# Optimization experiments

Hardware: AMD Instinct MI355X
Metric: run time of the kernel (lower is better)

The kernel has to match this reference:

```python
import jax, jax.numpy as jnp
import numpy as np

B = 64          # number of jets
LVLS = 13       # tree levels (complete binary tree, 4096 leaves/jet)
F = 7           # input features
H = 64          # hidden size
SIZES = [B * (2 ** j) for j in range(LVLS)]
OFFS = np.concatenate([[0], np.cumsum(SIZES)])  # level offsets into flat contents


def setup_inputs() -> dict:
    key = jax.random.key(0)
    ks = jax.random.split(key, 9)
    n_total = int(OFFS[-1])  # 524224
    s = lambda k, shp, fan: jax.random.normal(k, shp, jnp.float32) / np.sqrt(fan)
    return {
        "contents": jax.random.normal(ks[0], (n_total, F), jnp.float32),
        "W_u": s(ks[1], (H, F), F),       "b_u": jnp.zeros((H,), jnp.float32),
        "W_r": s(ks[2], (3 * H, 3 * H), 3 * H), "b_r": jnp.zeros((3 * H,), jnp.float32),
        "W_h": s(ks[3], (H, 3 * H), 3 * H),     "b_h": jnp.zeros((H,), jnp.float32),
        "W_z": s(ks[4], (4 * H, 4 * H), 4 * H), "b_z": jnp.zeros((4 * H,), jnp.float32),
    }


def reference(contents, W_u, b_u, W_r, b_r, W_h, b_h, W_z, b_z):
    # Bottom-up recursive gated embedding (n_iters=0 path -> relu activation).
    up = None  # embedding of level j+1
    for j in reversed(range(LVLS)):
        c = contents[int(OFFS[j]):int(OFFS[j + 1])]        # [n_j, F]
        u = jax.nn.relu(c @ W_u.T + b_u)                   # [n_j, H]
        if j == LVLS - 1:
            up = u                                         # leaf level: no inners
            continue
        n = SIZES[j]
        # children of node k are (2k, 2k+1) at level j+1 -> strided gather
        h_L = up[0::2]                                     # [n_j, H]
        h_R = up[1::2]                                     # [n_j, H]
        hhu = jnp.concatenate([h_L, h_R, u], axis=1)       # [n_j, 3H]
        r = jax.nn.sigmoid(hhu @ W_r.T + b_r)              # reset gate
        h_H = jax.nn.relu((r * hhu) @ W_h.T + b_h)         # candidate
        z = jnp.concatenate([h_H, hhu], axis=1) @ W_z.T + b_z  # [n_j, 4H]
        g = jax.nn.softmax(z.reshape(n, 4, H), axis=1)     # softmax over 4 gates
        up = g[:, 0] * h_H + g[:, 1] * h_L + g[:, 2] * h_R + g[:, 3] * u
    return up.reshape(B, -1)                               # [B, H]
```

## Files before the change

kernel.cpp:

```cpp
#include <hip/hip_runtime.h>
#include <hip/hip_bf16.h>


#define LOG2E 1.4426950408889634f
#define OSTR 76

typedef __bf16 bf16x8 __attribute__((ext_vector_type(8)));
typedef unsigned short u16x8 __attribute__((ext_vector_type(8)));
typedef float f32x4 __attribute__((ext_vector_type(4)));
typedef unsigned short bfr;

__device__ __forceinline__ float bfr2f(bfr v) { return __uint_as_float(((unsigned)v) << 16); }
__device__ __forceinline__ bfr f2bfr(float f) {
    __hip_bfloat16 h = __float2bfloat16(f);
    return __builtin_bit_cast(bfr, h);
}
__device__ __forceinline__ float fexp2(float x) {
#if __has_builtin(__builtin_amdgcn_exp2f)
    return __builtin_amdgcn_exp2f(x);
#else
    return exp2f(x);
#endif
}
__device__ __forceinline__ float frcp(float x) {
#if __has_builtin(__builtin_amdgcn_rcpf)
    return __builtin_amdgcn_rcpf(x);
#else
    return 1.f / x;
#endif
}

__device__ __forceinline__ int fidx(int Mt, int kt, int q, int ln, int KT) {
    return ((((Mt * KT + kt) * 4 + q) * 16 + ln) * 8);
}

__device__ __host__ __forceinline__ size_t lvloff(int j) {
    return (size_t)((64 << j) - 64) * 64;
}

__device__ __forceinline__ void pack_one(const float* __restrict__ W, bfr* __restrict__ dst,
                                         int d, int K, float scale) {
    int KT = K >> 5;
    int j = d & 7, lnc = (d >> 3) & 15, q = (d >> 7) & 3;
    int t1 = d >> 9;
    int kt = t1 % KT, ntile = t1 / KT;
    int ncol = ntile * 16 + lnc;
    int k = kt * 32 + q * 8 + j;
    dst[d] = f2bfr(W[(size_t)ncol * K + k] * scale);
}

__global__ void convert_weights(const float* __restrict__ Wr, const float* __restrict__ Wh,
                                const float* __restrict__ Wz, const float* __restrict__ Wu,
                                const float* __restrict__ br, const float* __restrict__ bz,
                                bfr* __restrict__ wr, bfr* __restrict__ wh, bfr* __restrict__ wz,
                                bfr* __restrict__ wu,
                                float* __restrict__ brs, float* __restrict__ bzs) {
    int i = blockIdx.x * 256 + threadIdx.x;
    if (i < 36864) pack_one(Wr, wr, i, 192, LOG2E);
    if (i < 12288) pack_one(Wh, wh, i, 192, 1.f);
    if (i < 65536) pack_one(Wz, wz, i, 256, LOG2E);
    if (i < 2048) {
        int j = i & 7, lnc = (i >> 3) & 15, q = (i >> 7) & 3, ntile = i >> 9;
        int k = q * 8 + j, ncol = ntile * 16 + lnc;
        wu[i] = (k < 7) ? f2bfr(Wu[ncol * 7 + k]) : (bfr)0;
    }
    if (i < 192) brs[i] = br[i] * LOG2E;
    if (i < 256) bzs[i] = bz[i] * LOG2E;
}

__device__ __forceinline__ void stage_c(const float* __restrict__ csrc, int rows,
                                        bfr* s_c) {
    const int tid = threadIdx.x;
    for (int t = tid; t < rows * 4; t += 256) {
        int row = t >> 2, qg = t & 3;
        ushort v[8] = {0, 0, 0, 0, 0, 0, 0, 0};
        if (qg == 0) {
            const float* cp = csrc + (size_t)row * 7;
#pragma unroll
            for (int k = 0; k < 7; ++k) v[k] = f2bfr(cp[k]);
        }
        *(uint4*)&s_c[(((row >> 4) * 4 + qg) * 16 + (row & 15)) * 8] = *(const uint4*)v;
    }
}

__device__ __forceinline__ bf16x8 load_c_frag(const float* __restrict__ c,
                                              size_t grow, bool active) {
    u16x8 cv = {0, 0, 0, 0, 0, 0, 0, 0};
    if (active) {
        const float* cp = c + grow * 7;
#pragma unroll
        for (int k = 0; k < 7; ++k) cv[k] = f2bfr(cp[k]);
    }
    return __builtin_bit_cast(bf16x8, cv);
}

__device__ __forceinline__ void store_up_coalesced(
    int row0, int rows, bfr* __restrict__ u_io,
    const ushort (&ovv)[4][4], int Mtn, bfr* s_t)
{
    const int tid = threadIdx.x;
    const int lane = tid & 63, w = tid >> 6;
    const int ln = lane & 15, q = lane >> 4;
    const int colbase = w * 16 + q * 4;
    __syncthreads();
#pragma unroll
    for (int Mt = 0; Mt < 4; ++Mt) {
        if (Mt < Mtn) {
            int row = Mt * 16 + ln;
            if (row < rows)
                *(uint2*)&s_t[row * OSTR + colbase] = *(const uint2*)ovv[Mt];
        }
    }
    __syncthreads();
#pragma unroll
    for (int it = 0; it < 2; ++it) {
        int idx = it * 256 + tid;
        int row = idx >> 3, ck = idx & 7;
        if (row < rows)
            *(uint4*)&u_io[(size_t)(row0 + row) * 64 + ck * 8] =
                *(const uint4*)&s_t[row * OSTR + ck * 8];
    }
}

__device__ __forceinline__ void mmu_own(const bfr* s_c, bfr* s_hhu, bf16x8 awu,
                                        f32x4 bu4, int Mtn, int ln, int q,
                                        int colbase) {
#pragma unroll
    for (int Mt = 0; Mt < 4; ++Mt) {
        if (Mt < Mtn) {
            bf16x8 Bc = *(const bf16x8*)&s_c[((Mt * 4 + q) * 16 + ln) * 8];
            f32x4 acc = {0.f, 0.f, 0.f, 0.f};
            acc = __builtin_amdgcn_mfma_f32_16x16x32_bf16(awu, Bc, acc, 0, 0, 0);
            int kk = 128 + colbase;
            int addr = fidx(Mt, kk >> 5, (kk >> 3) & 3, ln, 6) + (kk & 7);
            ushort uv[4];
#pragma unroll
            for (int r = 0; r < 4; ++r) uv[r] = f2bfr(fmaxf(acc[r] + bu4[r], 0.f));
            *(uint2*)&s_hhu[addr] = *(const uint2*)uv;
        }
    }
}

template <bool CHILD_U>
__device__ __forceinline__ void tile_glob(
    int row0,
    const bfr* __restrict__ ch, const float* __restrict__ c_child,
    const float* __restrict__ c_own, bfr* __restrict__ u_io,
    const bfr* __restrict__ wu, const float* __restrict__ b_u,
    const bfr* __restrict__ wr, const float* __restrict__ brs,
    const bfr* __restrict__ wh, const float* __restrict__ b_h,
    const bfr* __restrict__ wz, const float* __restrict__ bzs,
    bfr* s_hhu, bfr* s_t)
{
    bfr* s_hH = s_t;
    const int tid = threadIdx.x;
    const int lane = tid & 63, w = tid >> 6;
    const int ln = lane & 15, q = lane >> 4;
    const int colbase = w * 16 + q * 4;

    if (!CHILD_U) {
#pragma unroll
        for (int it = 0; it < 4; ++it) {
            int idx = it * 256 + tid;
            int lns = idx & 15, qs = (idx >> 4) & 3, kts = (idx >> 6) & 3, Mts = idx >> 8;
            int row = Mts * 16 + lns;
            int k = kts * 32 + qs * 8;
            const bfr* src = (k < 64)
                ? ch + (size_t)(2 * (row0 + row)) * 64 + k
                : ch + (size_t)(2 * (row0 + row) + 1) * 64 + (k - 64);
            *(uint4*)&s_hhu[fidx(Mts, kts, qs, lns, 6)] = *(const uint4*)src;
        }
    } else {
        stage_c(c_child + (size_t)(2 * row0) * 7, 128, s_t + 2048);
    }
    stage_c(c_own + (size_t)row0 * 7, 64, s_t);
    __syncthreads();

    {
        bf16x8 awu = *(const bf16x8*)&wu[fidx(w, 0, q, ln, 1)];
        f32x4 bu4 = *(const f32x4*)&b_u[colbase];
        if (CHILD_U) {
#pragma unroll
            for (int Mt = 0; Mt < 8; ++Mt) {
                bf16x8 Bc = *(const bf16x8*)&s_t[2048 + (((Mt * 4 + q) * 16 + ln) * 8)];
                f32x4 acc = {0.f, 0.f, 0.f, 0.f};
                acc = __builtin_amdgcn_mfma_f32_16x16x32_bf16(awu, Bc, acc, 0, 0, 0);
                int crow = Mt * 16 + ln;
                int row = crow >> 1;
                int kk = (crow & 1) * 64 + colbase;
                int addr = fidx(row >> 4, kk >> 5, (kk >> 3) & 3, row & 15, 6) + (kk & 7);
                ushort uv[4];
#pragma unroll
                for (int r = 0; r < 4; ++r) uv[r] = f2bfr(fmaxf(acc[r] + bu4[r], 0.f));
                *(uint2*)&s_hhu[addr] = *(const uint2*)uv;
            }
        }
        mmu_own(s_t, s_hhu, awu, bu4, 4, ln, q, colbase);
    }
    __syncthreads();

    {
        bf16x8 Af[3][6];
#pragma unroll
        for (int nt = 0; nt < 3; ++nt)
#pragma unroll
            for (int kt = 0; kt < 6; ++kt)
                Af[nt][kt] = *(const bf16x8*)&wr[fidx(w * 3 + nt, kt, q, ln, 6)];
#pragma unroll
        for (int Mt = 0; Mt < 4; ++Mt) {
            bf16x8 Bf[6];
#pragma unroll
            for (int kt = 0; kt < 6; ++kt)
                Bf[kt] = *(const bf16x8*)&s_hhu[fidx(Mt, kt, q, ln, 6)];
#pragma unroll
            for (int nt = 0; nt < 3; ++nt) {
                int cb1 = (w * 3 + nt) * 16 + q * 4;
                f32x4 acc = {0.f, 0.f, 0.f, 0.f};
#pragma unroll
                for (int kt = 0; kt < 6; ++kt)
                    acc = __builtin_amdgcn_mfma_f32_16x16x32_bf16(Af[nt][kt], Bf[kt], acc, 0, 0, 0);
                f32x4 br4 = *(const f32x4*)&brs[cb1];
                int addr = fidx(Mt, cb1 >> 5, (cb1 >> 3) & 3, ln, 6) + (cb1 & 7);
                ushort hh[4], tt[4];
                *(uint2*)hh = *(const uint2*)&s_hhu[addr];
#pragma unroll
                for (int r = 0; r < 4; ++r) {
                    float e = fexp2(-(acc[r] + br4[r]));
                    tt[r] = f2bfr(frcp(1.f + e) * bfr2f(hh[r]));
                }
                *(uint2*)&s_t[addr] = *(const uint2*)tt;
            }
        }
    }
    __syncthreads();

    f32x4 hacc[4];
    {
        bf16x8 Ah[6];
#pragma unroll
        for (int kt = 0; kt < 6; ++kt)
            Ah[kt] = *(const bf16x8*)&wh[fidx(w, kt, q, ln, 6)];
#pragma unroll
        for (int Mt = 0; Mt < 4; ++Mt) {
            f32x4 acc = {0.f, 0.f, 0.f, 0.f};
#pragma unroll
            for (int kt = 0; kt < 6; ++kt) {
                bf16x8 Bf = *(const bf16x8*)&s_t[fidx(Mt, kt, q, ln, 6)];
                acc = __builtin_amdgcn_mfma_f32_16x16x32_bf16(Ah[kt], Bf, acc, 0, 0, 0);
            }
            hacc[Mt] = acc;
        }
    }
    __syncthreads();
    {
        f32x4 bh4 = *(const f32x4*)&b_h[colbase];
#pragma unroll
        for (int Mt = 0; Mt < 4; ++Mt) {
            int addr = fidx(Mt, colbase >> 5, (colbase >> 3) & 3, ln, 2) + (colbase & 7);
            ushort hv[4];
#pragma unroll
            for (int r = 0; r < 4; ++r) hv[r] = f2bfr(fmaxf(hacc[Mt][r] + bh4[r], 0.f));
            *(uint2*)&s_hH[addr] = *(const uint2*)hv;
        }
    }
    __syncthreads();

    {
        f32x4 az[4][4];
#pragma unroll
        for (int Mt = 0; Mt < 4; ++Mt)
#pragma unroll
            for (int g = 0; g < 4; ++g) az[Mt][g] = (f32x4){0.f, 0.f, 0.f, 0.f};
#pragma unroll
        for (int g = 0; g < 4; ++g) {
            bf16x8 Aw[8];
#pragma unroll
            for (int kt = 0; kt < 8; ++kt)
                Aw[kt] = *(const bf16x8*)&wz[fidx(g * 4 + w, kt, q, ln, 8)];
#pragma unroll
            for (int Mt = 0; Mt < 4; ++Mt) {
                f32x4 acc = az[Mt][g];
                acc = __builtin_amdgcn_mfma_f32_16x16x32_bf16(
                    Aw[0], *(const bf16x8*)&s_hH[fidx(Mt, 0, q, ln, 2)], acc, 0, 0, 0);
                acc = __builtin_amdgcn_mfma_f32_16x16x32_bf16(
                    Aw[1], *(const bf16x8*)&s_hH[fidx(Mt, 1, q, ln, 2)], acc, 0, 0, 0);
#pragma unroll
                for (int kt = 0; kt < 6; ++kt)
                    acc = __builtin_amdgcn_mfma_f32_16x16x32_bf16(
                        Aw[2 + kt], *(const bf16x8*)&s_hhu[fidx(Mt, kt, q, ln, 6)], acc, 0, 0, 0);
                az[Mt][g] = acc;
            }
        }
        f32x4 bz0 = *(const f32x4*)&bzs[colbase];
        f32x4 bz1 = *(const f32x4*)&bzs[64 + colbase];
        f32x4 bz2 = *(const f32x4*)&bzs[128 + colbase];
        f32x4 bz3 = *(const f32x4*)&bzs[192 + colbase];
        ushort ovv[4][4];
#pragma unroll
        for (int Mt = 0; Mt < 4; ++Mt) {
            int aH = fidx(Mt, colbase >> 5, (colbase >> 3) & 3, ln, 2) + (colbase & 7);
            int a0 = fidx(Mt, colbase >> 5, (colbase >> 3) & 3, ln, 6) + (colbase & 7);
            int c1 = 64 + colbase, c2 = 128 + colbase;
            int a1 = fidx(Mt, c1 >> 5, (c1 >> 3) & 3, ln, 6) + (c1 & 7);
            int a2 = fidx(Mt, c2 >> 5, (c2 >> 3) & 3, ln, 6) + (c2 & 7);
            ushort hHv[4], u0[4], u1[4], u2[4];
            *(uint2*)hHv = *(const uint2*)&s_hH[aH];
            *(uint2*)u0 = *(const uint2*)&s_hhu[a0];
            *(uint2*)u1 = *(const uint2*)&s_hhu[a1];
            *(uint2*)u2 = *(const uint2*)&s_hhu[a2];
#pragma unroll
            for (int r = 0; r < 4; ++r) {
                float e0 = fexp2(az[Mt][0][r] + bz0[r]);
                float e1 = fexp2(az[Mt][1][r] + bz1[r]);
                float e2 = fexp2(az[Mt][2][r] + bz2[r]);
                float e3 = fexp2(az[Mt][3][r] + bz3[r]);
                float inv = frcp(e0 + e1 + e2 + e3);
                float v = (e0 * bfr2f(hHv[r]) + e1 * bfr2f(u0[r]) +
                           e2 * bfr2f(u1[r]) + e3 * bfr2f(u2[r])) * inv;
                ovv[Mt][r] = f2bfr(v);
            }
        }
        store_up_coalesced(row0, 64, u_io, ovv, 4, s_t);
    }
}

__global__ __launch_bounds__(256, 2) void level11_kernel(
    const float* __restrict__ c12, const float* __restrict__ c11,
    bfr* __restrict__ u_io,
    const bfr* __restrict__ wr, const float* __restrict__ brs,
    const bfr* __restrict__ wh, const float* __restrict__ b_h,
    const bfr* __restrict__ wz, const float* __restrict__ bzs,
    const bfr* __restrict__ wu, const float* __restrict__ b_u)
{
    __shared__ bfr s_hhu[12288];
    __shared__ bfr s_t[12288];
    tile_glob<true>(blockIdx.x * 64, nullptr, c12, c11, u_io,
                    wu, b_u, wr, brs, wh, b_h, wz, bzs, s_hhu, s_t);
}

__global__ __launch_bounds__(256, 2) void level_kernel(
    const bfr* __restrict__ ch, const float* __restrict__ c_own,
    bfr* __restrict__ u_io,
    const bfr* __restrict__ wr, const float* __restrict__ brs,
    const bfr* __restrict__ wh, const float* __restrict__ b_h,
    const bfr* __restrict__ wz, const float* __restrict__ bzs,
    const bfr* __restrict__ wu, const float* __restrict__ b_u)
{
    __shared__ bfr s_hhu[12288];
    __shared__ bfr s_t[12288];
    tile_glob<false>(blockIdx.x * 64, ch, nullptr, c_own, u_io,
                     wu, b_u, wr, brs, wh, b_h, wz, bzs, s_hhu, s_t);
}

__device__ __forceinline__ void load_wregs(
    const bfr* __restrict__ wr, const bfr* __restrict__ wh, const bfr* __restrict__ wz,
    const bfr* __restrict__ wu, int w, int q, int ln,
    bf16x8 (&Af)[3][6], bf16x8 (&Ah)[6], bf16x8 (&Aw)[4][8], bf16x8& awu)
{
#pragma unroll
    for (int nt = 0; nt < 3; ++nt)
#pragma unroll
        for (int kt = 0; kt < 6; ++kt)
            Af[nt][kt] = *(const bf16x8*)&wr[fidx(w * 3 + nt, kt, q, ln, 6)];
#pragma unroll
    for (int kt = 0; kt < 6; ++kt)
        Ah[kt] = *(const bf16x8*)&wh[fidx(w, kt, q, ln, 6)];
#pragma unroll
    for (int g = 0; g < 4; ++g)
#pragma unroll
        for (int kt = 0; kt < 8; ++kt)
            Aw[g][kt] = *(const bf16x8*)&wz[fidx(g * 4 + w, kt, q, ln, 8)];
    awu = *(const bf16x8*)&wu[fidx(w, 0, q, ln, 1)];
}

__device__ __forceinline__ void tile_regs(
    int row0, int rows,
    const bfr* __restrict__ ch, const float* __restrict__ c_own,
    bfr* __restrict__ u_io,
    const bf16x8 awu, const float* __restrict__ b_u,
    const bf16x8 (&Af)[3][6], const bf16x8 (&Ah)[6], const bf16x8 (&Aw)[4][8],
    const float* __restrict__ brs, const float* __restrict__ b_h,
    const float* __restrict__ bzs,
    float* __restrict__ outp, bfr* s_hhu, bfr* s_t, bfr* s_hH)
{
    const int tid = threadIdx.x;
    const int lane = tid & 63, w = tid >> 6;
    const int ln = lane & 15, q = lane >> 4;
    const int Mtn = (rows + 15) >> 4;
    const int colbase = w * 16 + q * 4;

    __syncthreads();

#pragma unroll
    for (int it = 0; it < 4; ++it) {
        int idx = it * 256 + tid;
        int lns = idx & 15, qs = (idx >> 4) & 3, kts = (idx >> 6) & 3, Mts = idx >> 8;
        int row = Mts * 16 + lns;
        if (row < rows) {
            int k = kts * 32 + qs * 8;
            const bfr* src = (k < 64)
                ? ch + (size_t)(2 * (row0 + row)) * 64 + k
                : ch + (size_t)(2 * (row0 + row) + 1) * 64 + (k - 64);
            *(uint4*)&s_hhu[fidx(Mts, kts, qs, lns, 6)] = *(const uint4*)src;
        }
    }
    {
        f32x4 bu4 = *(const f32x4*)&b_u[colbase];
#pragma unroll
        for (int Mt = 0; Mt < 4; ++Mt) {
            if (Mt < Mtn) {
                int row = Mt * 16 + ln;
                bf16x8 Bc = load_c_frag(c_own, (size_t)row0 + row, q == 0 && row < rows);
                f32x4 acc = {0.f, 0.f, 0.f, 0.f};
                acc = __builtin_amdgcn_mfma_f32_16x16x32_bf16(awu, Bc, acc, 0, 0, 0);
                int kk = 128 + colbase;
                int addr = fidx(Mt, kk >> 5, (kk >> 3) & 3, ln, 6) + (kk & 7);
                ushort uv[4];
#pragma unroll
                for (int r = 0; r < 4; ++r) uv[r] = f2bfr(fmaxf(acc[r] + bu4[r], 0.f));
                *(uint2*)&s_hhu[addr] = *(const uint2*)uv;
            }
        }
    }
    __syncthreads();

#pragma unroll
    for (int Mt = 0; Mt < 4; ++Mt) {
        if (Mt < Mtn) {
            bf16x8 Bf[6];
#pragma unroll
            for (int kt = 0; kt < 6; ++kt)
                Bf[kt] = *(const bf16x8*)&s_hhu[fidx(Mt, kt, q, ln, 6)];
#pragma unroll
            for (int nt = 0; nt < 3; ++nt) {
                int cb1 = (w * 3 + nt) * 16 + q * 4;
                f32x4 acc = {0.f, 0.f, 0.f, 0.f};
#pragma unroll
                for (int kt = 0; kt < 6; ++kt)
                    acc = __builtin_amdgcn_mfma_f32_16x16x32_bf16(Af[nt][kt], Bf[kt], acc, 0, 0, 0);
                f32x4 br4 = *(const f32x4*)&brs[cb1];
                int addr = fidx(Mt, cb1 >> 5, (cb1 >> 3) & 3, ln, 6) + (cb1 & 7);
                ushort hh[4], tt[4];
                *(uint2*)hh = *(const uint2*)&s_hhu[addr];
#pragma unroll
                for (int r = 0; r < 4; ++r) {
                    float e = fexp2(-(acc[r] + br4[r]));
                    tt[r] = f2bfr(frcp(1.f + e) * bfr2f(hh[r]));
                }
                *(uint2*)&s_t[addr] = *(const uint2*)tt;
            }
        }
    }
    __syncthreads();

    {
        f32x4 bh4 = *(const f32x4*)&b_h[colbase];
#pragma unroll
        for (int Mt = 0; Mt < 4; ++Mt) {
            if (Mt < Mtn) {
                f32x4 acc = {0.f, 0.f, 0.f, 0.f};
#pragma unroll
                for (int kt = 0; kt < 6; ++kt) {
                    bf16x8 Bf = *(const bf16x8*)&s_t[fidx(Mt, kt, q, ln, 6)];
                    acc = __builtin_amdgcn_mfma_f32_16x16x32_bf16(Ah[kt], Bf, acc, 0, 0, 0);
                }
                int addr = fidx(Mt, colbase >> 5, (colbase >> 3) & 3, ln, 2) + (colbase & 7);
                ushort hv[4];
#pragma unroll
                for (int r = 0; r < 4; ++r) hv[r] = f2bfr(fmaxf(acc[r] + bh4[r], 0.f));
                *(uint2*)&s_hH[addr] = *(const uint2*)hv;
            }
        }
    }
    __syncthreads();

    {
        f32x4 bz0 = *(const f32x4*)&bzs[colbase];
        f32x4 bz1 = *(const f32x4*)&bzs[64 + colbase];
        f32x4 bz2 = *(const f32x4*)&bzs[128 + colbase];
        f32x4 bz3 = *(const f32x4*)&bzs[192 + colbase];
#pragma unroll
        for (int Mt = 0; Mt < 4; ++Mt) {
            if (Mt < Mtn) {
                bf16x8 Az[8];
                Az[0] = *(const bf16x8*)&s_hH[fidx(Mt, 0, q, ln, 2)];
                Az[1] = *(const bf16x8*)&s_hH[fidx(Mt, 1, q, ln, 2)];
#pragma unroll
                for (int kt = 0; kt < 6; ++kt)
                    Az[2 + kt] = *(const bf16x8*)&s_hhu[fidx(Mt, kt, q, ln, 6)];
                f32x4 azg[4];
#pragma unroll
                for (int g = 0; g < 4; ++g) {
                    f32x4 acc = {0.f, 0.f, 0.f, 0.f};
#pragma unroll
                    for (int kt = 0; kt < 8; ++kt)
                        acc = __builtin_amdgcn_mfma_f32_16x16x32_bf16(Aw[g][kt], Az[kt], acc, 0, 0, 0);
                    azg[g] = acc;
                }
                int row = Mt * 16 + ln;
                if (row < rows) {
                    int aH = fidx(Mt, colbase >> 5, (colbase >> 3) & 3, ln, 2) + (colbase & 7);
                    int a0 = fidx(Mt, colbase >> 5, (colbase >> 3) & 3, ln, 6) + (colbase & 7);
                    int c1 = 64 + colbase, c2 = 128 + colbase;
                    int a1 = fidx(Mt, c1 >> 5, (c1 >> 3) & 3, ln, 6) + (c1 & 7);
                    int a2 = fidx(Mt, c2 >> 5, (c2 >> 3) & 3, ln, 6) + (c2 & 7);
                    ushort hHv[4], u0[4], u1[4], u2[4], ov[4];
                    *(uint2*)hHv = *(const uint2*)&s_hH[aH];
                    *(uint2*)u0 = *(const uint2*)&s_hhu[a0];
                    *(uint2*)u1 = *(const uint2*)&s_hhu[a1];
                    *(uint2*)u2 = *(const uint2*)&s_hhu[a2];
                    float of[4];
#pragma unroll
                    for (int r = 0; r < 4; ++r) {
                        float e0 = fexp2(azg[0][r] + bz0[r]);
                        float e1 = fexp2(azg[1][r] + bz1[r]);
                        float e2 = fexp2(azg[2][r] + bz2[r]);
                        float e3 = fexp2(azg[3][r] + bz3[r]);
                        float inv = frcp(e0 + e1 + e2 + e3);
                        float v = (e0 * bfr2f(hHv[r]) + e1 * bfr2f(u0[r]) +
                                   e2 * bfr2f(u1[r]) + e3 * bfr2f(u2[r])) * inv;
                        ov[r] = f2bfr(v); of[r] = v;
                    }
                    *(uint2*)&s_t[row * OSTR + colbase] = *(const uint2*)ov;
                    if (outp)
                        *(float4*)&outp[(size_t)(row0 + row) * 64 + colbase] = *(const float4*)of;
                }
            }
        }
    }
    __syncthreads();
    {
        const int tid2 = threadIdx.x;
#pragma unroll
        for (int it = 0; it < 2; ++it) {
            int idx = it * 256 + tid2;
            int row = idx >> 3, ck = idx & 7;
            if (row < rows)
                *(uint4*)&u_io[(size_t)(row0 + row) * 64 + ck * 8] =
                    *(const uint4*)&s_t[row * OSTR + ck * 8];
        }
    }
}

__global__ __launch_bounds__(256, 1) void fused_mid_regs(
    const float* __restrict__ contents, bfr* __restrict__ u_all,
    const bfr* __restrict__ wr, const float* __restrict__ brs,
    const bfr* __restrict__ wh, const float* __restrict__ b_h,
    const bfr* __restrict__ wz, const float* __restrict__ bzs,
    const bfr* __restrict__ wu, const float* __restrict__ b_u)
{
    __shared__ bfr s_hhu[12288];
    __shared__ bfr s_t[12288];
    __shared__ bfr s_hH[4096];
    const int tid = threadIdx.x;
    const int lane = tid & 63, w = tid >> 6, ln = lane & 15, q = lane >> 4;
    bf16x8 Af[3][6], Ah[6], Aw[4][8], awu;
    load_wregs(wr, wh, wz, wu, w, q, ln, Af, Ah, Aw, awu);
    for (int j = 8; j >= 2; --j) {
        int rows = 1 << (j - 2);
        const float* c_own = contents + (size_t)((64 << j) - 64) * 7;
        tile_regs(blockIdx.x * rows, rows,
                  u_all + lvloff(j + 1), c_own, u_all + lvloff(j),
                  awu, b_u, Af, Ah, Aw, brs, b_h, bzs,
                  nullptr, s_hhu, s_t, s_hH);
    }
}

__global__ __launch_bounds__(256, 1) void fused_tail_regs(
    const float* __restrict__ contents, bfr* __restrict__ u_all,
    const bfr* __restrict__ wr, const float* __restrict__ brs,
    const bfr* __restrict__ wh, const float* __restrict__ b_h,
    const bfr* __restrict__ wz, const float* __restrict__ bzs,
    const bfr* __restrict__ wu, const float* __restrict__ b_u,
    float* __restrict__ outp)
{
    __shared__ bfr s_hhu[12288];
    __shared__ bfr s_t[12288];
    __shared__ bfr s_hH[4096];
    const int tid = threadIdx.x;
    const int lane = tid & 63, w = tid >> 6, ln = lane & 15, q = lane >> 4;
    bf16x8 Af[3][6], Ah[6], Aw[4][8], awu;
    load_wregs(wr, wh, wz, wu, w, q, ln, Af, Ah, Aw, awu);
    for (int j = 1; j >= 0; --j) {
        int rows = 1 << j;
        const float* c_own = contents + (size_t)((64 << j) - 64) * 7;
        tile_regs(blockIdx.x * rows, rows,
                  u_all + lvloff(j + 1), c_own, u_all + lvloff(j),
                  awu, b_u, Af, Ah, Aw, brs, b_h, bzs,
                  (j == 0) ? outp : nullptr, s_hhu, s_t, s_hH);
    }
}

extern "C" void kernel_launch(void* const* d_in, const int* in_sizes, int n_in,
                              void* d_out, int out_size, void* d_ws, size_t ws_size,
                              hipStream_t stream) {
    const float* contents = (const float*)d_in[0];
    const float* W_u = (const float*)d_in[1];
    const float* b_u = (const float*)d_in[2];
    const float* W_r = (const float*)d_in[3];
    const float* b_r = (const float*)d_in[4];
    const float* W_h = (const float*)d_in[5];
    const float* b_h = (const float*)d_in[6];
    const float* W_z = (const float*)d_in[7];
    const float* b_z = (const float*)d_in[8];
    float* out = (float*)d_out;

    bfr* u_all = (bfr*)d_ws;
    bfr* wr = u_all + (size_t)524224 * 64;
    bfr* wh = wr + 36864;
    bfr* wz = wh + 12288;
    float* brs = (float*)(wz + 65536);
    float* bzs = brs + 192;
    bfr* wu = (bfr*)(bzs + 256);

    convert_weights<<<256, 256, 0, stream>>>(W_r, W_h, W_z, W_u, b_r, b_z,
                                             wr, wh, wz, wu, brs, bzs);

    const float* c12 = contents + (size_t)((64 << 12) - 64) * 7;
    const float* c11 = contents + (size_t)((64 << 11) - 64) * 7;
    const float* c10 = contents + (size_t)((64 << 10) - 64) * 7;
    const float* c9  = contents + (size_t)((64 << 9) - 64) * 7;

    level11_kernel<<<2048, 256, 0, stream>>>(c12, c11, u_all + lvloff(11),
                                             wr, brs, wh, b_h, wz, bzs, wu, b_u);
    level_kernel<<<1024, 256, 0, stream>>>(u_all + lvloff(11), c10, u_all + lvloff(10),
                                           wr, brs, wh, b_h, wz, bzs, wu, b_u);
    level_kernel<<<512, 256, 0, stream>>>(u_all + lvloff(10), c9, u_all + lvloff(9),
                                          wr, brs, wh, b_h, wz, bzs, wu, b_u);
    fused_mid_regs<<<256, 256, 0, stream>>>(contents, u_all,
                                            wr, brs, wh, b_h, wz, bzs, wu, b_u);
    fused_tail_regs<<<64, 256, 0, stream>>>(contents, u_all,
                                            wr, brs, wh, b_h, wz, bzs, wu, b_u, out);
}
```

Measured before the change: 195.5 us.

## Prefetch weights and contents into registers; chain tree levels through LDS

In tile_glob, the node's own contents are now loaded straight into registers and converted to MFMA fragments. This removes the LDS staging and its barrier, and the W_r/W_h loads are hoisted so they issue earlier. The W_z gate weights are double-buffered, so the next gate's fragments load while the current gate's MFMAs run. In the fused mid/tail kernels, levels after the first read child embeddings from the previous level's LDS output tile instead of global memory. They also skip the intermediate global store, keeping only the final one. The trade-off is higher register pressure and a dependence on each block owning exactly the children it needs.

```diff
diff --git a/kernel.cpp b/kernel.cpp
--- a/kernel.cpp
+++ b/kernel.cpp
@@ -122,25 +122,6 @@
     }
 }
 
-__device__ __forceinline__ void mmu_own(const bfr* s_c, bfr* s_hhu, bf16x8 awu,
-                                        f32x4 bu4, int Mtn, int ln, int q,
-                                        int colbase) {
-#pragma unroll
-    for (int Mt = 0; Mt < 4; ++Mt) {
-        if (Mt < Mtn) {
-            bf16x8 Bc = *(const bf16x8*)&s_c[((Mt * 4 + q) * 16 + ln) * 8];
-            f32x4 acc = {0.f, 0.f, 0.f, 0.f};
-            acc = __builtin_amdgcn_mfma_f32_16x16x32_bf16(awu, Bc, acc, 0, 0, 0);
-            int kk = 128 + colbase;
-            int addr = fidx(Mt, kk >> 5, (kk >> 3) & 3, ln, 6) + (kk & 7);
-            ushort uv[4];
-#pragma unroll
-            for (int r = 0; r < 4; ++r) uv[r] = f2bfr(fmaxf(acc[r] + bu4[r], 0.f));
-            *(uint2*)&s_hhu[addr] = *(const uint2*)uv;
-        }
-    }
-}
-
 template <bool CHILD_U>
 __device__ __forceinline__ void tile_glob(
     int row0,
@@ -158,7 +139,41 @@
     const int ln = lane & 15, q = lane >> 4;
     const int colbase = w * 16 + q * 4;
 
-    if (!CHILD_U) {
+    float cof[4][7];
+#pragma unroll
+    for (int Mt = 0; Mt < 4; ++Mt) {
+        const float* cp = c_own + (size_t)(row0 + Mt * 16 + ln) * 7;
+#pragma unroll
+        for (int k = 0; k < 7; ++k) cof[Mt][k] = (q == 0) ? cp[k] : 0.f;
+    }
+    bf16x8 awu = *(const bf16x8*)&wu[fidx(w, 0, q, ln, 1)];
+    bf16x8 Af[3][6];
+#pragma unroll
+    for (int nt = 0; nt < 3; ++nt)
+#pragma unroll
+        for (int kt = 0; kt < 6; ++kt)
+            Af[nt][kt] = *(const bf16x8*)&wr[fidx(w * 3 + nt, kt, q, ln, 6)];
+
+    f32x4 bu4 = *(const f32x4*)&b_u[colbase];
+
+    if (CHILD_U) {
+        stage_c(c_child + (size_t)(2 * row0) * 7, 128, s_t + 2048);
+        __syncthreads();
+#pragma unroll
+        for (int Mt = 0; Mt < 8; ++Mt) {
+            bf16x8 Bc = *(const bf16x8*)&s_t[2048 + (((Mt * 4 + q) * 16 + ln) * 8)];
+            f32x4 acc = {0.f, 0.f, 0.f, 0.f};
+            acc = __builtin_amdgcn_mfma_f32_16x16x32_bf16(awu, Bc, acc, 0, 0, 0);
+            int crow = Mt * 16 + ln;
+            int row = crow >> 1;
+            int kk = (crow & 1) * 64 + colbase;
+            int addr = fidx(row >> 4, kk >> 5, (kk >> 3) & 3, row & 15, 6) + (kk & 7);
+            ushort uv[4];
+#pragma unroll
+            for (int r = 0; r < 4; ++r) uv[r] = f2bfr(fmaxf(acc[r] + bu4[r], 0.f));
+            *(uint2*)&s_hhu[addr] = *(const uint2*)uv;
+        }
+    } else {
 #pragma unroll
         for (int it = 0; it < 4; ++it) {
             int idx = it * 256 + tid;
@@ -170,42 +185,32 @@
                 : ch + (size_t)(2 * (row0 + row) + 1) * 64 + (k - 64);
             *(uint4*)&s_hhu[fidx(Mts, kts, qs, lns, 6)] = *(const uint4*)src;
         }
-    } else {
-        stage_c(c_child + (size_t)(2 * row0) * 7, 128, s_t + 2048);
-    }
-    stage_c(c_own + (size_t)row0 * 7, 64, s_t);
-    __syncthreads();
-
-    {
-        bf16x8 awu = *(const bf16x8*)&wu[fidx(w, 0, q, ln, 1)];
-        f32x4 bu4 = *(const f32x4*)&b_u[colbase];
-        if (CHILD_U) {
-#pragma unroll
-            for (int Mt = 0; Mt < 8; ++Mt) {
-                bf16x8 Bc = *(const bf16x8*)&s_t[2048 + (((Mt * 4 + q) * 16 + ln) * 8)];
-                f32x4 acc = {0.f, 0.f, 0.f, 0.f};
-                acc = __builtin_amdgcn_mfma_f32_16x16x32_bf16(awu, Bc, acc, 0, 0, 0);
-                int crow = Mt * 16 + ln;
-                int row = crow >> 1;
-                int kk = (crow & 1) * 64 + colbase;
-                int addr = fidx(row >> 4, kk >> 5, (kk >> 3) & 3, row & 15, 6) + (kk & 7);
-                ushort uv[4];
-#pragma unroll
-                for (int r = 0; r < 4; ++r) uv[r] = f2bfr(fmaxf(acc[r] + bu4[r], 0.f));
-                *(uint2*)&s_hhu[addr] = *(const uint2*)uv;
-            }
-        }
-        mmu_own(s_t, s_hhu, awu, bu4, 4, ln, q, colbase);
-    }
-    __syncthreads();
-
-    {
-        bf16x8 Af[3][6];
-#pragma unroll
-        for (int nt = 0; nt < 3; ++nt)
-#pragma unroll
-            for (int kt = 0; kt < 6; ++kt)
-                Af[nt][kt] = *(const bf16x8*)&wr[fidx(w * 3 + nt, kt, q, ln, 6)];
+    }
+
+#pragma unroll
+    for (int Mt = 0; Mt < 4; ++Mt) {
+        u16x8 cv = {0, 0, 0, 0, 0, 0, 0, 0};
+        if (q == 0) {
+#pragma unroll
+            for (int k = 0; k < 7; ++k) cv[k] = f2bfr(cof[Mt][k]);
+        }
+        bf16x8 Bc = __builtin_bit_cast(bf16x8, cv);
+        f32x4 acc = {0.f, 0.f, 0.f, 0.f};
+        acc = __builtin_amdgcn_mfma_f32_16x16x32_bf16(awu, Bc, acc, 0, 0, 0);
+        int kk = 128 + colbase;
+        int addr = fidx(Mt, kk >> 5, (kk >> 3) & 3, ln, 6) + (kk & 7);
+        ushort uv[4];
+#pragma unroll
+        for (int r = 0; r < 4; ++r) uv[r] = f2bfr(fmaxf(acc[r] + bu4[r], 0.f));
+        *(uint2*)&s_hhu[addr] = *(const uint2*)uv;
+    }
+    __syncthreads();
+
+    bf16x8 Ah[6];
+#pragma unroll
+    for (int kt = 0; kt < 6; ++kt)
+        Ah[kt] = *(const bf16x8*)&wh[fidx(w, kt, q, ln, 6)];
+    {
 #pragma unroll
         for (int Mt = 0; Mt < 4; ++Mt) {
             bf16x8 Bf[6];
@@ -234,12 +239,12 @@
     }
     __syncthreads();
 
+    bf16x8 Awc[8], Awn[8];
+#pragma unroll
+    for (int kt = 0; kt < 8; ++kt)
+        Awc[kt] = *(const bf16x8*)&wz[fidx(0 * 4 + w, kt, q, ln, 8)];
     f32x4 hacc[4];
     {
-        bf16x8 Ah[6];
-#pragma unroll
-        for (int kt = 0; kt < 6; ++kt)
-            Ah[kt] = *(const bf16x8*)&wh[fidx(w, kt, q, ln, 6)];
 #pragma unroll
         for (int Mt = 0; Mt < 4; ++Mt) {
             f32x4 acc = {0.f, 0.f, 0.f, 0.f};
@@ -268,27 +273,28 @@
     {
         f32x4 az[4][4];
 #pragma unroll
-        for (int Mt = 0; Mt < 4; ++Mt)
-#pragma unroll
-            for (int g = 0; g < 4; ++g) az[Mt][g] = (f32x4){0.f, 0.f, 0.f, 0.f};
-#pragma unroll
         for (int g = 0; g < 4; ++g) {
-            bf16x8 Aw[8];
-#pragma unroll
-            for (int kt = 0; kt < 8; ++kt)
-                Aw[kt] = *(const bf16x8*)&wz[fidx(g * 4 + w, kt, q, ln, 8)];
+            if (g < 3) {
+#pragma unroll
+                for (int kt = 0; kt < 8; ++kt)
+                    Awn[kt] = *(const bf16x8*)&wz[fidx((g + 1) * 4 + w, kt, q, ln, 8)];
+            }
 #pragma unroll
             for (int Mt = 0; Mt < 4; ++Mt) {
-                f32x4 acc = az[Mt][g];
+                f32x4 acc = {0.f, 0.f, 0.f, 0.f};
                 acc = __builtin_amdgcn_mfma_f32_16x16x32_bf16(
-                    Aw[0], *(const bf16x8*)&s_hH[fidx(Mt, 0, q, ln, 2)], acc, 0, 0, 0);
+                    Awc[0], *(const bf16x8*)&s_hH[fidx(Mt, 0, q, ln, 2)], acc, 0, 0, 0);
                 acc = __builtin_amdgcn_mfma_f32_16x16x32_bf16(
-                    Aw[1], *(const bf16x8*)&s_hH[fidx(Mt, 1, q, ln, 2)], acc, 0, 0, 0);
+                    Awc[1], *(const bf16x8*)&s_hH[fidx(Mt, 1, q, ln, 2)], acc, 0, 0, 0);
 #pragma unroll
                 for (int kt = 0; kt < 6; ++kt)
                     acc = __builtin_amdgcn_mfma_f32_16x16x32_bf16(
-                        Aw[2 + kt], *(const bf16x8*)&s_hhu[fidx(Mt, kt, q, ln, 6)], acc, 0, 0, 0);
+                        Awc[2 + kt], *(const bf16x8*)&s_hhu[fidx(Mt, kt, q, ln, 6)], acc, 0, 0, 0);
                 az[Mt][g] = acc;
+            }
+            if (g < 3) {
+#pragma unroll
+                for (int kt = 0; kt < 8; ++kt) Awc[kt] = Awn[kt];
             }
         }
         f32x4 bz0 = *(const f32x4*)&bzs[colbase];
@@ -373,6 +379,7 @@
     awu = *(const bf16x8*)&wu[fidx(w, 0, q, ln, 1)];
 }
 
+template <bool CH_LDS, bool STORE_U>
 __device__ __forceinline__ void tile_regs(
     int row0, int rows,
     const bfr* __restrict__ ch, const float* __restrict__ c_own,
@@ -398,10 +405,16 @@
         int row = Mts * 16 + lns;
         if (row < rows) {
             int k = kts * 32 + qs * 8;
-            const bfr* src = (k < 64)
-                ? ch + (size_t)(2 * (row0 + row)) * 64 + k
-                : ch + (size_t)(2 * (row0 + row) + 1) * 64 + (k - 64);
-            *(uint4*)&s_hhu[fidx(Mts, kts, qs, lns, 6)] = *(const uint4*)src;
+            if (CH_LDS) {
+                int crow = 2 * row + (k >= 64 ? 1 : 0);
+                *(uint4*)&s_hhu[fidx(Mts, kts, qs, lns, 6)] =
+                    *(const uint4*)&s_t[crow * OSTR + (k & 63)];
+            } else {
+                const bfr* src = (k < 64)
+                    ? ch + (size_t)(2 * (row0 + row)) * 64 + k
+                    : ch + (size_t)(2 * (row0 + row) + 1) * 64 + (k - 64);
+                *(uint4*)&s_hhu[fidx(Mts, kts, qs, lns, 6)] = *(const uint4*)src;
+            }
         }
     }
     {
@@ -528,8 +541,8 @@
             }
         }
     }
-    __syncthreads();
-    {
+    if (STORE_U) {
+        __syncthreads();
         const int tid2 = threadIdx.x;
 #pragma unroll
         for (int it = 0; it < 2; ++it) {
@@ -556,13 +569,27 @@
     const int lane = tid & 63, w = tid >> 6, ln = lane & 15, q = lane >> 4;
     bf16x8 Af[3][6], Ah[6], Aw[4][8], awu;
     load_wregs(wr, wh, wz, wu, w, q, ln, Af, Ah, Aw, awu);
-    for (int j = 8; j >= 2; --j) {
+    {
+        const float* c8 = contents + (size_t)((64 << 8) - 64) * 7;
+        tile_regs<false, false>(blockIdx.x * 64, 64,
+                                u_all + lvloff(9), c8, u_all + lvloff(8),
+                                awu, b_u, Af, Ah, Aw, brs, b_h, bzs,
+                                nullptr, s_hhu, s_t, s_hH);
+    }
+    for (int j = 7; j >= 3; --j) {
         int rows = 1 << (j - 2);
         const float* c_own = contents + (size_t)((64 << j) - 64) * 7;
-        tile_regs(blockIdx.x * rows, rows,
-                  u_all + lvloff(j + 1), c_own, u_all + lvloff(j),
-                  awu, b_u, Af, Ah, Aw, brs, b_h, bzs,
-                  nullptr, s_hhu, s_t, s_hH);
+        tile_regs<true, false>(blockIdx.x * rows, rows,
+                               nullptr, c_own, u_all + lvloff(j),
+                               awu, b_u, Af, Ah, Aw, brs, b_h, bzs,
+                               nullptr, s_hhu, s_t, s_hH);
+    }
+    {
+        const float* c2 = contents + (size_t)((64 << 2) - 64) * 7;
+        tile_regs<true, true>(blockIdx.x, 1,
+                              nullptr, c2, u_all + lvloff(2),
+                              awu, b_u, Af, Ah, Aw, brs, b_h, bzs,
+                              nullptr, s_hhu, s_t, s_hH);
     }
 }
 
@@ -581,13 +608,19 @@
     const int lane = tid & 63, w = tid >> 6, ln = lane & 15, q = lane >> 4;
     bf16x8 Af[3][6], Ah[6], Aw[4][8], awu;
     load_wregs(wr, wh, wz, wu, w, q, ln, Af, Ah, Aw, awu);
-    for (int j = 1; j >= 0; --j) {
-        int rows = 1 << j;
-        const float* c_own = contents + (size_t)((64 << j) - 64) * 7;
-        tile_regs(blockIdx.x * rows, rows,
-                  u_all + lvloff(j + 1), c_own, u_all + lvloff(j),
-                  awu, b_u, Af, Ah, Aw, brs, b_h, bzs,
-                  (j == 0) ? outp : nullptr, s_hhu, s_t, s_hH);
+    {
+        const float* c1 = contents + (size_t)((64 << 1) - 64) * 7;
+        tile_regs<false, false>(blockIdx.x * 2, 2,
+                                u_all + lvloff(2), c1, u_all + lvloff(1),
+                                awu, b_u, Af, Ah, Aw, brs, b_h, bzs,
+                                nullptr, s_hhu, s_t, s_hH);
+    }
+    {
+        const float* c0 = contents;
+        tile_regs<true, false>(blockIdx.x, 1,
+                               nullptr, c0, u_all + lvloff(0),
+                               awu, b_u, Af, Ah, Aw, brs, b_h, bzs,
+                               outp, s_hhu, s_t, s_hH);
     }
 }
 
```

Measured after the change: 210.6 us. +7.7%, slower.
